# Performance work log

Hardware: AMD Instinct MI355X
Metric: run time of the kernel (lower is better)

Reference implementation:

```python
import jax, jax.numpy as jnp
import numpy as np

B, S, D = 2, 2048, 1024
H, KD, VD = 16, 64, 64


def setup_inputs() -> dict:
    key = jax.random.key(0)
    ks = jax.random.split(key, 12)
    s = 1.0 / np.sqrt(D)
    return {
        "q": jax.random.normal(ks[0], (B, S, D), jnp.float32),
        "k": jax.random.normal(ks[1], (B, S, D), jnp.float32),
        "v": jax.random.normal(ks[2], (B, S, D), jnp.float32),
        "mask": jnp.ones((S, S), jnp.int32),
        "Wq": jax.random.normal(ks[3], (D, H * KD), jnp.float32) * s,
        "bq": jnp.zeros((H * KD,), jnp.float32),
        "Wk": jax.random.normal(ks[4], (D, H * KD), jnp.float32) * s,
        "bk": jnp.zeros((H * KD,), jnp.float32),
        "Wv": jax.random.normal(ks[5], (D, H * VD), jnp.float32) * s,
        "bv": jnp.zeros((H * VD,), jnp.float32),
        "Wo": jax.random.normal(ks[6], (H * VD, D), jnp.float32) * (1.0 / np.sqrt(H * VD)),
        "bo": jnp.zeros((D,), jnp.float32),
    }


def reference(q, k, v, mask, Wq, bq, Wk, bk, Wv, bv, Wo, bo):
    bs = q.shape[0]
    # projections -> [B, H, S, d]
    qh = (q @ Wq + bq).reshape(bs, -1, H, KD).transpose(0, 2, 1, 3)
    kh = (k @ Wk + bk).reshape(bs, -1, H, KD).transpose(0, 2, 1, 3)
    vh = (v @ Wv + bv).reshape(bs, -1, H, VD).transpose(0, 2, 1, 3)
    scores = jnp.einsum("bhqd,bhkd->bhqk", qh, kh) / np.sqrt(KD)
    scores = jnp.where(mask[None, None, :, :] == 0, -1e9, scores)
    probs = jax.nn.softmax(scores, axis=-1)  # dropout is identity in eval
    attn = jnp.einsum("bhqk,bhkd->bhqd", probs, vh)
    concat = attn.transpose(0, 2, 1, 3).reshape(bs, -1, H * VD)
    return concat @ Wo + bo
```

## Files before the change

kernel.cpp:

```cpp
#include <hip/hip_runtime.h>
#include <stdint.h>

typedef __attribute__((ext_vector_type(8))) short short8;
typedef __attribute__((ext_vector_type(4))) float f32x4;
typedef __attribute__((ext_vector_type(16))) float f32x16;
typedef __attribute__((ext_vector_type(2))) unsigned int u32x2;

constexpr int Bc = 2, Sc = 2048, Dc = 1024, Hc = 16;
constexpr int MR = Bc * Sc;
#define CSC 0.18033688011112042f

static __device__ __forceinline__ unsigned short f2bf(float f) {
    union { float f; uint32_t u; } v; v.f = f;
    uint32_t u = v.u;
    u += 0x7FFFu + ((u >> 16) & 1u);
    return (unsigned short)(u >> 16);
}

static __device__ __forceinline__ uint32_t cvtpk(float lo, float hi) {
    uint32_t r;
    asm("v_cvt_pk_bf16_f32 %0, %1, %2" : "=v"(r) : "v"(lo), "v"(hi));
    return r;
}

static __device__ __forceinline__ float exp2a(float x) {
    float r;
    asm("v_exp_f32 %0, %1" : "=v"(r) : "v"(x));
    return r;
}

static __device__ __forceinline__ void gload_lds16(const void* g, void* l) {
    __builtin_amdgcn_global_load_lds(
        (const __attribute__((address_space(1))) unsigned int*)g,
        (__attribute__((address_space(3))) unsigned int*)l, 16, 0, 0);
}

__global__ void transpose_w_kernel(const float* __restrict__ Wq, const float* __restrict__ Wk,
                                   const float* __restrict__ Wv, const float* __restrict__ Wo,
                                   unsigned short* __restrict__ out) {
    __shared__ unsigned short tile[64][65];
    const float* W = (blockIdx.z == 0) ? Wq : (blockIdx.z == 1) ? Wk
                   : (blockIdx.z == 2) ? Wv : Wo;
    unsigned short* Wt = out + (size_t)blockIdx.z * (size_t)Dc * Dc;
    int n0 = blockIdx.x * 64, k0 = blockIdx.y * 64;
    int c = threadIdx.x & 63, r0 = threadIdx.x >> 6;
#pragma unroll
    for (int rr = 0; rr < 16; rr++) {
        int r = r0 + rr * 4;
        tile[r][c] = f2bf(W[(size_t)(k0 + r) * Dc + n0 + c]);
    }
    __syncthreads();
#pragma unroll
    for (int rr = 0; rr < 16; rr++) {
        int r = r0 + rr * 4;
        Wt[(size_t)(n0 + r) * Dc + k0 + c] = tile[c][r];
    }
}

__global__ __launch_bounds__(256, 2)
void gemm_qkv_kernel(const float* __restrict__ Xq, const float* __restrict__ Xk,
                     const float* __restrict__ Xv,
                     const unsigned short* __restrict__ Wt,
                     const float* __restrict__ bq, const float* __restrict__ bk,
                     const float* __restrict__ bv,
                     unsigned short* __restrict__ Qp,
                     unsigned short* __restrict__ Kp,
                     unsigned short* __restrict__ Vt)
{
    __shared__ unsigned short POOL[16384];
    unsigned short* Alds = POOL;
    unsigned short* Blds = POOL + 8192;
    const int lane = threadIdx.x & 63;
    const int wave = threadIdx.x >> 6;
    const int g = lane >> 4, r = lane & 15;
    const int wr = wave >> 1, wc = wave & 1;
    const int tM = blockIdx.x * 128, tN = blockIdx.y * 128;
    const int m_blk = tN >> 10;
    const float* Af = (m_blk == 0) ? Xq : (m_blk == 1) ? Xk : Xv;
    const float* bias = (m_blk == 0) ? bq : (m_blk == 1) ? bk : bv;

    f32x4 acc[4][4] = {};

    const float* asrc[4];
#pragma unroll
    for (int i = 0; i < 4; i++) {
        int c = wave * 4 + i;
        int row = c * 8 + (lane >> 3);
        asrc[i] = Af + (size_t)(tM + row) * 1024 + (lane & 7) * 8;
    }

    float4 afA[4][2];
#pragma unroll
    for (int i = 0; i < 4; i++) {
        afA[i][0] = *(const float4*)(asrc[i]);
        afA[i][1] = *(const float4*)(asrc[i] + 4);
    }

    for (int kt = 0; kt < 1024; kt += 64) {
#pragma unroll
        for (int i = 0; i < 4; i++) {
            int c = wave * 4 + i;
            int row = c * 8 + (lane >> 3);
            gload_lds16(Wt + (size_t)(tN + row) * 1024 + kt + (lane & 7) * 8,
                        (void*)(Blds + c * 512));
        }
        __builtin_amdgcn_sched_barrier(0);

#pragma unroll
        for (int i = 0; i < 4; i++) {
            int c = wave * 4 + i;
            union { uint32_t u[4]; short8 s; } pk;
            pk.u[0] = cvtpk(afA[i][0].x, afA[i][0].y);
            pk.u[1] = cvtpk(afA[i][0].z, afA[i][0].w);
            pk.u[2] = cvtpk(afA[i][1].x, afA[i][1].y);
            pk.u[3] = cvtpk(afA[i][1].z, afA[i][1].w);
            *(short8*)(Alds + c * 512 + lane * 8) = pk.s;
        }
        if (kt < 960) {
#pragma unroll
            for (int i = 0; i < 4; i++) {
                afA[i][0] = *(const float4*)(asrc[i] + kt + 64);
                afA[i][1] = *(const float4*)(asrc[i] + kt + 68);
            }
        }
        __builtin_amdgcn_sched_barrier(0);
        if (kt < 960) {
            asm volatile("s_waitcnt vmcnt(8) lgkmcnt(0)" ::: "memory");
        } else {
            asm volatile("s_waitcnt vmcnt(0) lgkmcnt(0)" ::: "memory");
        }
        __builtin_amdgcn_s_barrier();
        __builtin_amdgcn_sched_barrier(0);

#pragma unroll
        for (int ks = 0; ks < 2; ks++) {
            short8 av[4], bvv[4];
#pragma unroll
            for (int mf = 0; mf < 4; mf++)
                av[mf] = *(const short8*)(Alds + (wr * 64 + mf * 16 + r) * 64 + ks * 32 + g * 8);
#pragma unroll
            for (int nf = 0; nf < 4; nf++)
                bvv[nf] = *(const short8*)(Blds + (wc * 64 + nf * 16 + r) * 64 + ks * 32 + g * 8);
#pragma unroll
            for (int mf = 0; mf < 4; mf++)
#pragma unroll
                for (int nf = 0; nf < 4; nf++)
                    acc[mf][nf] = __builtin_amdgcn_mfma_f32_16x16x32_bf16(av[mf], bvv[nf], acc[mf][nf], 0, 0, 0);
        }
        __builtin_amdgcn_sched_barrier(0);
        asm volatile("s_waitcnt lgkmcnt(0)" ::: "memory");
        __builtin_amdgcn_s_barrier();
        __builtin_amdgcn_sched_barrier(0);
    }

    const int cbase = (tN & 1023) + wc * 64;
    const int h = cbase >> 6;
    const int bblk = tM >> 11;
    const int tMs = tM & 2047;
    unsigned short* Ow = POOL + wave * 2304;
    const float scl = (m_blk == 0) ? CSC : 1.0f;

    if (m_blk < 2) {
        unsigned short* dstQ = (m_blk == 0) ? Qp : Kp;
#pragma unroll
        for (int p = 0; p < 2; p++) {
#pragma unroll
            for (int mf2 = 0; mf2 < 2; mf2++)
#pragma unroll
                for (int nf = 0; nf < 4; nf++)
#pragma unroll
                    for (int i = 0; i < 4; i++) {
                        float val = (acc[2 * p + mf2][nf][i] + bias[cbase + nf * 16 + r]) * scl;
                        Ow[(mf2 * 16 + g * 4 + i) * 72 + nf * 16 + r] = f2bf(val);
                    }
            asm volatile("s_waitcnt lgkmcnt(0)" ::: "memory");
#pragma unroll
            for (int r4 = 0; r4 < 4; r4++) {
                int sl = r4 * 8 + (lane >> 3), dc = (lane & 7) * 8;
                short8 vv = *(const short8*)(Ow + sl * 72 + dc);
                int s = tMs + wr * 64 + p * 32 + sl;
                *(short8*)(dstQ + (((size_t)(bblk * Hc + h)) * Sc + s) * 64 + dc) = vv;
            }
            asm volatile("s_waitcnt lgkmcnt(0)" ::: "memory");
        }
    } else {
#pragma unroll
        for (int p = 0; p < 2; p++) {
#pragma unroll
            for (int nf2 = 0; nf2 < 2; nf2++)
#pragma unroll
                for (int mf = 0; mf < 4; mf++)
#pragma unroll
                    for (int i = 0; i < 4; i++) {
                        float val = acc[mf][2 * p + nf2][i] + bias[cbase + (2 * p + nf2) * 16 + r];
                        Ow[(nf2 * 16 + r) * 72 + mf * 16 + g * 4 + i] = f2bf(val);
                    }
            asm volatile("s_waitcnt lgkmcnt(0)" ::: "memory");
#pragma unroll
            for (int r4 = 0; r4 < 4; r4++) {
                int dl = r4 * 8 + (lane >> 3), sc_ = (lane & 7) * 8;
                short8 vv = *(const short8*)(Ow + dl * 72 + sc_);
                int dk = p * 32 + dl;
                *(short8*)(Vt + ((size_t)(bblk * Hc + h) * 64 + dk) * Sc
                              + (tMs + wr * 64 + sc_)) = vv;
            }
            asm volatile("s_waitcnt lgkmcnt(0)" ::: "memory");
        }
    }
}

__global__ __launch_bounds__(256, 2)
void gemm_out_kernel(const unsigned short* __restrict__ A,
                     const unsigned short* __restrict__ Bt,
                     const float* __restrict__ bias,
                     float* __restrict__ Cout)
{
    __shared__ unsigned short Alds[128 * 64];
    __shared__ unsigned short Blds[128 * 64];
    const int lane = threadIdx.x & 63;
    const int wave = threadIdx.x >> 6;
    const int g = lane >> 4, r = lane & 15;
    const int wr = wave >> 1, wc = wave & 1;
    const int tM = blockIdx.x * 128, tN = blockIdx.y * 128;

    f32x4 acc[4][4] = {};

    for (int kt = 0; kt < 1024; kt += 64) {
        __syncthreads();
#pragma unroll
        for (int i = 0; i < 4; i++) {
            int c = wave * 4 + i;
            int row = c * 8 + (lane >> 3);
            int kcol = kt + (lane & 7) * 8;
            gload_lds16(A  + (size_t)(tM + row) * 1024 + kcol, (void*)(Alds + c * 512));
            gload_lds16(Bt + (size_t)(tN + row) * 1024 + kcol, (void*)(Blds + c * 512));
        }
        __syncthreads();
#pragma unroll
        for (int ks = 0; ks < 2; ks++) {
            short8 av[4], bvv[4];
#pragma unroll
            for (int mf = 0; mf < 4; mf++)
                av[mf] = *(const short8*)(Alds + (wr * 64 + mf * 16 + r) * 64 + ks * 32 + g * 8);
#pragma unroll
            for (int nf = 0; nf < 4; nf++)
                bvv[nf] = *(const short8*)(Blds + (wc * 64 + nf * 16 + r) * 64 + ks * 32 + g * 8);
#pragma unroll
            for (int mf = 0; mf < 4; mf++)
#pragma unroll
                for (int nf = 0; nf < 4; nf++)
                    acc[mf][nf] = __builtin_amdgcn_mfma_f32_16x16x32_bf16(av[mf], bvv[nf], acc[mf][nf], 0, 0, 0);
        }
    }

#pragma unroll
    for (int mf = 0; mf < 4; mf++)
#pragma unroll
      for (int nf = 0; nf < 4; nf++)
#pragma unroll
        for (int i = 0; i < 4; i++) {
            int row = tM + wr * 64 + mf * 16 + g * 4 + i;
            int col = tN + wc * 64 + nf * 16 + r;
            Cout[(size_t)row * 1024 + col] = acc[mf][nf][i] + bias[col];
        }
}

__global__ __launch_bounds__(512, 4)
void attn_kernel(const unsigned short* __restrict__ Qp,
                 const unsigned short* __restrict__ Kp,
                 const unsigned short* __restrict__ Vt,
                 unsigned short* __restrict__ Oc)
{
    __shared__ __align__(16) unsigned short SH[2][3][64 * 72];

    const int tid = threadIdx.x;
    const int wave = tid >> 6, lane = tid & 63;
    const int ql = lane & 31, h5 = lane >> 5;
    const int half = wave >> 2;
    const int bh = blockIdx.y;
    const int qbw = blockIdx.x * 128 + (wave & 3) * 32;

    const unsigned short* Kg = Kp + (size_t)bh * Sc * 64 + (size_t)half * 1024 * 64;
    const unsigned short* Vg = Vt + (size_t)bh * (size_t)64 * Sc + half * 1024;

    const unsigned short* Qrow = Qp + ((size_t)bh * Sc + qbw + ql) * 64 + h5 * 8;
    short8 qf[4];
#pragma unroll
    for (int ks = 0; ks < 4; ks++) qf[ks] = *(const short8*)(Qrow + ks * 16);

    unsigned short* Kc = &SH[half][0][0];
    unsigned short* Kn = &SH[half][1][0];
    unsigned short* Vl = &SH[half][2][0];
    const int fro = ql * 72 + h5 * 8;

    const int t8 = tid & 255;
    const int srow = t8 >> 3, sc8 = (t8 & 7) * 8;
    const int stl = srow * 72 + sc8;
    const unsigned short* kgp = Kg + srow * 64 + sc8;
    const unsigned short* vg0 = Vg + (size_t)srow * Sc + sc8;
    const unsigned short* vg1 = Vg + (size_t)(32 + srow) * Sc + sc8;

    f32x16 ot0{}, ot1{};
    f32x16 st0{}, st1{};
    float lsum = 0.f;

    short8 ka = *(const short8*)(kgp);
    short8 kb2 = *(const short8*)(kgp + 2048);
    *(short8*)(Kc + stl) = ka;  *(short8*)(Kc + stl + 2304) = kb2;
    asm volatile("s_waitcnt lgkmcnt(0)" ::: "memory");
    __builtin_amdgcn_s_barrier();
    ka  = *(const short8*)(kgp + 4096);
    kb2 = *(const short8*)(kgp + 4096 + 2048);
    short8 va  = *(const short8*)(vg0);
    short8 vb2 = *(const short8*)(vg1);
    __builtin_amdgcn_s_setprio(1);
#pragma unroll
    for (int ks = 0; ks < 4; ks++) {
        short8 a0 = *(const short8*)(Kc + fro + ks * 16);
        st0 = __builtin_amdgcn_mfma_f32_32x32x16_bf16(a0, qf[ks], st0, 0, 0, 0);
        short8 a1 = *(const short8*)(Kc + fro + 2304 + ks * 16);
        st1 = __builtin_amdgcn_mfma_f32_32x32x16_bf16(a1, qf[ks], st1, 0, 0, 0);
    }
    __builtin_amdgcn_s_setprio(0);

    for (int t = 0; t < 16; ++t) {
        if (t < 15) { *(short8*)(Kn + stl) = ka;  *(short8*)(Kn + stl + 2304) = kb2; }
        *(short8*)(Vl + stl) = va;  *(short8*)(Vl + stl + 2304) = vb2;
        asm volatile("s_waitcnt lgkmcnt(0)" ::: "memory");
        __builtin_amdgcn_s_barrier();

        if (t < 14) {
            ka  = *(const short8*)(kgp + (t + 2) * 4096);
            kb2 = *(const short8*)(kgp + (t + 2) * 4096 + 2048);
        }
        if (t < 15) {
            va  = *(const short8*)(vg0 + (t + 1) * 64);
            vb2 = *(const short8*)(vg1 + (t + 1) * 64);
        }

        float ps = 0.f;
#pragma unroll
        for (int c4 = 0; c4 < 4; c4++) {
            const f32x16& sv = (c4 < 2) ? st0 : st1;
            const int s8 = (c4 & 1) * 8;
            float e0 = exp2a(sv[s8 + 0]), e1 = exp2a(sv[s8 + 1]);
            float e2 = exp2a(sv[s8 + 2]), e3 = exp2a(sv[s8 + 3]);
            float e4 = exp2a(sv[s8 + 4]), e5 = exp2a(sv[s8 + 5]);
            float e6 = exp2a(sv[s8 + 6]), e7 = exp2a(sv[s8 + 7]);
            ps += ((e0 + e1) + (e2 + e3)) + ((e4 + e5) + (e6 + e7));
            uint32_t c0 = cvtpk(e0, e1), c1 = cvtpk(e2, e3);
            uint32_t c2 = cvtpk(e4, e5), c3 = cvtpk(e6, e7);
            asm("v_permlane32_swap_b32 %0, %1" : "+v"(c0), "+v"(c2));
            asm("v_permlane32_swap_b32 %0, %1" : "+v"(c1), "+v"(c3));
            union { uint32_t u[4]; short8 s; } bf;
            bf.u[0] = c0; bf.u[1] = c1; bf.u[2] = c2; bf.u[3] = c3;
            __builtin_amdgcn_s_setprio(1);
            short8 a0 = *(const short8*)(Vl + fro + c4 * 16);
            ot0 = __builtin_amdgcn_mfma_f32_32x32x16_bf16(a0, bf.s, ot0, 0, 0, 0);
            short8 a1 = *(const short8*)(Vl + fro + 2304 + c4 * 16);
            ot1 = __builtin_amdgcn_mfma_f32_32x32x16_bf16(a1, bf.s, ot1, 0, 0, 0);
            __builtin_amdgcn_s_setprio(0);
        }
        ps += __shfl_xor(ps, 32);
        lsum += ps;

        if (t < 15) {
            st0 = f32x16{}; st1 = f32x16{};
            __builtin_amdgcn_s_setprio(1);
#pragma unroll
            for (int ks = 0; ks < 4; ks++) {
                short8 a0 = *(const short8*)(Kn + fro + ks * 16);
                st0 = __builtin_amdgcn_mfma_f32_32x32x16_bf16(a0, qf[ks], st0, 0, 0, 0);
                short8 a1 = *(const short8*)(Kn + fro + 2304 + ks * 16);
                st1 = __builtin_amdgcn_mfma_f32_32x32x16_bf16(a1, qf[ks], st1, 0, 0, 0);
            }
            __builtin_amdgcn_s_setprio(0);
        }

        __builtin_amdgcn_s_barrier();
        unsigned short* tswp = Kc; Kc = Kn; Kn = tswp;
    }

    float* Olds = (float*)&SH[0][0][0];
    float* Lld  = (float*)((char*)&SH[0][0][0] + 33792);
    __syncthreads();
    if (h5 == 0) Lld[wave * 32 + ql] = lsum;
    __syncthreads();
    float l2 = Lld[(wave ^ 4) * 32 + ql];
    if (wave >= 4) {
        float* dst = Olds + (size_t)(wave - 4) * (64 * 33) + ql;
#pragma unroll
        for (int i = 0; i < 16; i++) {
            int d0 = (i & 3) + 8 * (i >> 2) + 4 * h5;
            dst[d0 * 33]        = ot0[i];
            dst[(d0 + 32) * 33] = ot1[i];
        }
    }
    __syncthreads();
    if (wave < 4) {
        float inv = 1.0f / (lsum + l2);
        const float* src = Olds + (size_t)wave * (64 * 33) + ql;
#pragma unroll
        for (int i = 0; i < 16; i++) {
            int d0 = (i & 3) + 8 * (i >> 2) + 4 * h5;
            ot0[i] = (ot0[i] + src[d0 * 33]) * inv;
            ot1[i] = (ot1[i] + src[(d0 + 32) * 33]) * inv;
        }
        asm volatile("s_waitcnt lgkmcnt(0)" ::: "memory");
        __builtin_amdgcn_sched_barrier(0);
        unsigned short* Ost = (unsigned short*)(Olds + (size_t)wave * (64 * 33));
#pragma unroll
        for (int dt = 0; dt < 2; dt++)
#pragma unroll
            for (int t = 0; t < 4; t++) {
                const f32x16& o = dt ? ot1 : ot0;
                uint32_t w0 = cvtpk(o[4 * t + 0], o[4 * t + 1]);
                uint32_t w1 = cvtpk(o[4 * t + 2], o[4 * t + 3]);
                *(u32x2*)(Ost + ql * 72 + dt * 32 + t * 8 + h5 * 4) = u32x2{w0, w1};
            }
        asm volatile("s_waitcnt lgkmcnt(0)" ::: "memory");
        __builtin_amdgcn_sched_barrier(0);
        int r = lane >> 1, cb = (lane & 1) * 4;
        int b = bh >> 4, hh = bh & 15;
        unsigned short* dstg = Oc + ((size_t)b * Sc + qbw + r) * (Hc * 64) + hh * 64;
#pragma unroll
        for (int t = 0; t < 4; t++)
            *(short8*)(dstg + (cb + t) * 8) = *(const short8*)(Ost + r * 72 + (cb + t) * 8);
    }
}

extern "C" void kernel_launch(void* const* d_in, const int* in_sizes, int n_in,
                              void* d_out, int out_size, void* d_ws, size_t ws_size,
                              hipStream_t stream)
{
    (void)in_sizes; (void)n_in; (void)out_size; (void)ws_size;
    const float* q  = (const float*)d_in[0];
    const float* k  = (const float*)d_in[1];
    const float* v  = (const float*)d_in[2];
    const float* Wq = (const float*)d_in[4];
    const float* bq = (const float*)d_in[5];
    const float* Wk = (const float*)d_in[6];
    const float* bk = (const float*)d_in[7];
    const float* Wv = (const float*)d_in[8];
    const float* bv = (const float*)d_in[9];
    const float* Wo = (const float*)d_in[10];
    const float* bo = (const float*)d_in[11];

    char* ws = (char*)d_ws;
    unsigned short* Wt    = (unsigned short*)(ws);
    unsigned short* Qp    = (unsigned short*)(ws + (size_t)8  * 1024 * 1024);
    unsigned short* Kp    = (unsigned short*)(ws + (size_t)16 * 1024 * 1024);
    unsigned short* Vtg   = (unsigned short*)(ws + (size_t)24 * 1024 * 1024);
    unsigned short* attnC = (unsigned short*)(ws + (size_t)32 * 1024 * 1024);

    transpose_w_kernel<<<dim3(16, 16, 4), 256, 0, stream>>>(Wq, Wk, Wv, Wo, Wt);

    gemm_qkv_kernel<<<dim3(32, 24), 256, 0, stream>>>(q, k, v, Wt, bq, bk, bv, Qp, Kp, Vtg);

    attn_kernel<<<dim3(16, 32), 512, 0, stream>>>(Qp, Kp, Vtg, attnC);

    gemm_out_kernel<<<dim3(32, 8), 256, 0, stream>>>(attnC, Wt + 3 * 1048576, bo, (float*)d_out);
}
```

Baseline: 120.1 us.

## Double-buffer weight tiles in LDS and XOR-swizzle the LDS layout

The QKV projection GEMM now prefetches the next K-slice of the weight tile into a second LDS buffer while computing on the current one, and no longer waits on outstanding global loads before the barrier. A and B tiles are also stored with an XOR swizzle on the 16-byte chunk index, and the MFMA operand reads use the matching swizzle, to reduce LDS bank conflicts. This raises LDS use per block by half. It relies on the compiler's implicit wait for the register-loaded A data to also cover the earlier LDS-direct B loads, which is fragile.

```diff
diff --git a/kernel.cpp b/kernel.cpp
--- a/kernel.cpp
+++ b/kernel.cpp
@@ -67,12 +67,14 @@
                      unsigned short* __restrict__ Kp,
                      unsigned short* __restrict__ Vt)
 {
-    __shared__ unsigned short POOL[16384];
+    __shared__ unsigned short POOL[24576];
     unsigned short* Alds = POOL;
-    unsigned short* Blds = POOL + 8192;
+    unsigned short* Bl0  = POOL + 8192;
+    unsigned short* Bl1  = POOL + 16384;
     const int lane = threadIdx.x & 63;
     const int wave = threadIdx.x >> 6;
     const int g = lane >> 4, r = lane & 15;
+    const int r7 = r & 7;
     const int wr = wave >> 1, wc = wave & 1;
     const int tM = blockIdx.x * 128, tN = blockIdx.y * 128;
     const int m_blk = tN >> 10;
@@ -81,14 +83,22 @@
 
     f32x4 acc[4][4] = {};
 
+    const int lrow = lane >> 3, lun = lane & 7;
+    const int lswz = (lun ^ lrow) * 8;
     const float* asrc[4];
+    const unsigned short* bsrc[4];
 #pragma unroll
     for (int i = 0; i < 4; i++) {
         int c = wave * 4 + i;
-        int row = c * 8 + (lane >> 3);
-        asrc[i] = Af + (size_t)(tM + row) * 1024 + (lane & 7) * 8;
-    }
-
+        int row = c * 8 + lrow;
+        asrc[i] = Af + (size_t)(tM + row) * 1024 + lun * 8;
+        bsrc[i] = Wt + (size_t)(tN + row) * 1024 + lswz;
+    }
+
+#pragma unroll
+    for (int i = 0; i < 4; i++)
+        gload_lds16(bsrc[i], (void*)(Bl0 + (wave * 4 + i) * 512));
+    __builtin_amdgcn_sched_barrier(0);
     float4 afA[4][2];
 #pragma unroll
     for (int i = 0; i < 4; i++) {
@@ -96,13 +106,18 @@
         afA[i][1] = *(const float4*)(asrc[i] + 4);
     }
 
+    unsigned short* Bcur = Bl0;
+    unsigned short* Bnxt = Bl1;
+
+    int sw[2];
+    sw[0] = ((0 * 4 + g) ^ r7) * 8;
+    sw[1] = ((1 * 4 + g) ^ r7) * 8;
+
     for (int kt = 0; kt < 1024; kt += 64) {
-#pragma unroll
-        for (int i = 0; i < 4; i++) {
-            int c = wave * 4 + i;
-            int row = c * 8 + (lane >> 3);
-            gload_lds16(Wt + (size_t)(tN + row) * 1024 + kt + (lane & 7) * 8,
-                        (void*)(Blds + c * 512));
+        if (kt < 960) {
+#pragma unroll
+            for (int i = 0; i < 4; i++)
+                gload_lds16(bsrc[i] + kt + 64, (void*)(Bnxt + (wave * 4 + i) * 512));
         }
         __builtin_amdgcn_sched_barrier(0);
 
@@ -114,7 +129,7 @@
             pk.u[1] = cvtpk(afA[i][0].z, afA[i][0].w);
             pk.u[2] = cvtpk(afA[i][1].x, afA[i][1].y);
             pk.u[3] = cvtpk(afA[i][1].z, afA[i][1].w);
-            *(short8*)(Alds + c * 512 + lane * 8) = pk.s;
+            *(short8*)(Alds + c * 512 + lrow * 64 + lswz) = pk.s;
         }
         if (kt < 960) {
 #pragma unroll
@@ -124,11 +139,7 @@
             }
         }
         __builtin_amdgcn_sched_barrier(0);
-        if (kt < 960) {
-            asm volatile("s_waitcnt vmcnt(8) lgkmcnt(0)" ::: "memory");
-        } else {
-            asm volatile("s_waitcnt vmcnt(0) lgkmcnt(0)" ::: "memory");
-        }
+        asm volatile("s_waitcnt lgkmcnt(0)" ::: "memory");
         __builtin_amdgcn_s_barrier();
         __builtin_amdgcn_sched_barrier(0);
 
@@ -137,10 +148,10 @@
             short8 av[4], bvv[4];
 #pragma unroll
             for (int mf = 0; mf < 4; mf++)
-                av[mf] = *(const short8*)(Alds + (wr * 64 + mf * 16 + r) * 64 + ks * 32 + g * 8);
+                av[mf] = *(const short8*)(Alds + (wr * 64 + mf * 16 + r) * 64 + sw[ks]);
 #pragma unroll
             for (int nf = 0; nf < 4; nf++)
-                bvv[nf] = *(const short8*)(Blds + (wc * 64 + nf * 16 + r) * 64 + ks * 32 + g * 8);
+                bvv[nf] = *(const short8*)(Bcur + (wc * 64 + nf * 16 + r) * 64 + sw[ks]);
 #pragma unroll
             for (int mf = 0; mf < 4; mf++)
 #pragma unroll
@@ -151,6 +162,8 @@
         asm volatile("s_waitcnt lgkmcnt(0)" ::: "memory");
         __builtin_amdgcn_s_barrier();
         __builtin_amdgcn_sched_barrier(0);
+
+        unsigned short* tb = Bcur; Bcur = Bnxt; Bnxt = tb;
     }
 
     const int cbase = (tN & 1023) + wc * 64;
```

New measurement: 113.8 us. 1.06x faster.
